# Kernel optimization log

Hardware: AMD Instinct MI355X
Metric: run time of the kernel (lower is better)

## Reference

```python
import jax, jax.numpy as jnp
import numpy as np

B, SQ, SK, D, H = 4, 2048, 2048, 1024, 16
HD = D // H


def setup_inputs() -> dict:
    key = jax.random.key(0)
    ks = jax.random.split(key, 12)
    s = 1.0 / np.sqrt(D)
    return {
        "query": jax.random.normal(ks[0], (B, SQ, D), jnp.float32),
        "key": jax.random.normal(ks[1], (B, SK, D), jnp.float32),
        "value": jax.random.normal(ks[2], (B, SK, D), jnp.float32),
        "key_padding_mask": jax.random.randint(ks[3], (B, SK), 0, 2, jnp.int32),
        "Wq": jax.random.uniform(ks[4], (D, D), jnp.float32, -s, s),
        "bq": jnp.zeros((D,), jnp.float32),
        "Wk": jax.random.uniform(ks[5], (D, D), jnp.float32, -s, s),
        "bk": jnp.zeros((D,), jnp.float32),
        "Wv": jax.random.uniform(ks[6], (D, D), jnp.float32, -s, s),
        "bv": jnp.zeros((D,), jnp.float32),
        "Wo": jax.random.uniform(ks[7], (D, D), jnp.float32, -s, s),
        "bo": jnp.zeros((D,), jnp.float32),
    }


def reference(query, key, value, key_padding_mask, Wq, bq, Wk, bk, Wv, bv, Wo, bo):
    scale = HD ** -0.5
    # projections: torch Linear is x @ W.T + b
    q = (query @ Wq.T + bq).reshape(B, SQ, H, HD).transpose(0, 2, 1, 3)  # [B,H,SQ,HD]
    k = (key @ Wk.T + bk).reshape(B, SK, H, HD).transpose(0, 2, 1, 3)    # [B,H,SK,HD]
    v = (value @ Wv.T + bv).reshape(B, SK, H, HD).transpose(0, 2, 1, 3)  # [B,H,SK,HD]
    scores = jnp.einsum("bhqd,bhkd->bhqk", q, k) * scale                  # [B,H,SQ,SK]
    mask = key_padding_mask[:, None, None, :] != 0                        # True = keep
    scores = jnp.where(mask, scores, -jnp.inf)
    attn = jax.nn.softmax(scores, axis=-1)
    # dropout is identity at inference (eval mode)
    out = jnp.einsum("bhqk,bhkd->bhqd", attn, v)                          # [B,H,SQ,HD]
    out = out.transpose(0, 2, 1, 3).reshape(B, SQ, D)
    return out @ Wo.T + bo
```

## Files before the change

### kernel.cpp

```cpp
#include <hip/hip_runtime.h>


typedef __bf16 bf16_t;
typedef __attribute__((ext_vector_type(4))) __bf16 bf16x4;
typedef __attribute__((ext_vector_type(8))) __bf16 bf16x8;
typedef __attribute__((ext_vector_type(4))) float f32x4;

#define MFMA16(a, b, c) __builtin_amdgcn_mfma_f32_16x16x32_bf16(a, b, c, 0, 0, 0)

__device__ __forceinline__ void gl_lds16(const void* g, void* l) {
  __builtin_amdgcn_global_load_lds(
      (const __attribute__((address_space(1))) unsigned int*)g,
      (__attribute__((address_space(3))) unsigned int*)l, 16, 0, 0);
}

__global__ void wconv_kernel(const float* __restrict__ Wq, const float* __restrict__ Wk,
                             const float* __restrict__ Wv, const float* __restrict__ Wo,
                             bf16_t* __restrict__ out) {
  const int m = blockIdx.y;
  const float* src = (m == 0) ? Wq : (m == 1) ? Wk : (m == 2) ? Wv : Wo;
  bf16_t* dst = out + (size_t)m * (1024 * 1024);
  const int idx = (blockIdx.x * 256 + threadIdx.x) * 4;
  float4 v = *(const float4*)(src + idx);
  bf16x4 pk;
  pk[0] = (bf16_t)v.x; pk[1] = (bf16_t)v.y; pk[2] = (bf16_t)v.z; pk[3] = (bf16_t)v.w;
  *(bf16x4*)(dst + idx) = pk;
}

__global__ void iconv_kernel(const float* __restrict__ src, bf16_t* __restrict__ dst) {
  const size_t idx = ((size_t)blockIdx.x * 256 + threadIdx.x) * 4;
  float4 v = *(const float4*)(src + idx);
  bf16x4 pk;
  pk[0] = (bf16_t)v.x; pk[1] = (bf16_t)v.y; pk[2] = (bf16_t)v.z; pk[3] = (bf16_t)v.w;
  *(bf16x4*)(dst + idx) = pk;
}

__global__ __launch_bounds__(256, 2) void gemm_kernel(
    const bf16_t* __restrict__ A, const bf16_t* __restrict__ Bw,
    const float* __restrict__ bias, void* __restrict__ outp, const int out_mode) {
  __shared__ __align__(16) bf16_t As[2][16 * 512];
  __shared__ __align__(16) bf16_t Bs[2][16 * 512];

  const int tid = threadIdx.x;
  const int lane = tid & 63, wave = tid >> 6;
  const int fm = lane & 15, quad = lane >> 4;
  const int wr = wave >> 1, wc = wave & 1;
  const int m0 = blockIdx.x * 128, n0 = blockIdx.y * 128;

  f32x4 acc[4][4];
#pragma unroll
  for (int i = 0; i < 4; ++i)
#pragma unroll
    for (int j = 0; j < 4; ++j) acc[i][j] = f32x4{0.f, 0.f, 0.f, 0.f};

  auto stage = [&](int ks, int buf) {
    const int k0 = ks * 64;
#pragma unroll
    for (int it = 0; it < 4; ++it) {
      const int fid = wave * 4 + it;
      const int row = (fid >> 1) * 16 + fm;
      const int col = (fid & 1) * 32 + quad * 8;
      gl_lds16(A + (size_t)(m0 + row) * 1024 + k0 + col, As[buf] + fid * 512);
    }
#pragma unroll
    for (int it = 0; it < 4; ++it) {
      const int fid = wave * 4 + it;
      const int row = (fid >> 1) * 16 + fm;
      const int col = (fid & 1) * 32 + quad * 8;
      gl_lds16(Bw + (size_t)(n0 + row) * 1024 + k0 + col, Bs[buf] + fid * 512);
    }
  };

  stage(0, 0);
  for (int ks = 0; ks < 16; ++ks) {
    __syncthreads();
    if (ks + 1 < 16) stage(ks + 1, (ks + 1) & 1);
    const bf16_t* Ab = As[ks & 1];
    const bf16_t* Bb = Bs[ks & 1];
#pragma unroll
    for (int u = 0; u < 2; ++u) {
      bf16x8 af[4], bfr[4];
#pragma unroll
      for (int i = 0; i < 4; ++i)
        af[i] = *(const bf16x8*)(Ab + ((4 * wr + i) * 2 + u) * 512 + lane * 8);
#pragma unroll
      for (int j = 0; j < 4; ++j)
        bfr[j] = *(const bf16x8*)(Bb + ((4 * wc + j) * 2 + u) * 512 + lane * 8);
#pragma unroll
      for (int i = 0; i < 4; ++i)
#pragma unroll
        for (int j = 0; j < 4; ++j) acc[i][j] = MFMA16(af[i], bfr[j], acc[i][j]);
    }
  }

  float bval[4];
#pragma unroll
  for (int j = 0; j < 4; ++j) bval[j] = bias[n0 + wc * 64 + j * 16 + fm];

#pragma unroll
  for (int i = 0; i < 4; ++i) {
#pragma unroll
    for (int j = 0; j < 4; ++j) {
      const int col = n0 + wc * 64 + j * 16 + fm;
#pragma unroll
      for (int r = 0; r < 4; ++r) {
        const int row = m0 + wr * 64 + i * 16 + quad * 4 + r;
        const float v = acc[i][j][r] + bval[j];
        if (out_mode == 2) {
          ((float*)outp)[(size_t)row * 1024 + col] = v;
        } else if (out_mode == 0) {
          ((bf16_t*)outp)[(size_t)row * 1024 + col] = (bf16_t)v;
        } else {
          const int bb = row >> 11, sk = row & 2047;
          const int tt = sk >> 7, L128 = sk & 127;
          const int c = L128 >> 5, hf = (L128 >> 4) & 1;
          const int qd = (L128 >> 2) & 3, rr = L128 & 3;
          const int hh = col >> 6, hd = col & 63;
          const int nt = hd >> 4, fv = hd & 15;
          const size_t idx = (((size_t)(bb * 16 + hh)) << 17) + tt * 8192 +
                             (nt * 4 + c) * 512 + (qd * 16 + fv) * 8 + hf * 4 + rr;
          ((bf16_t*)outp)[idx] = (bf16_t)v;
        }
      }
    }
  }
}

__global__ __launch_bounds__(256, 2) void attn_kernel(
    const bf16_t* __restrict__ q16, const bf16_t* __restrict__ k16,
    const bf16_t* __restrict__ vt16, const int* __restrict__ mask,
    bf16_t* __restrict__ o16) {
  __shared__ __align__(16) bf16_t Kb[2][8192];
  __shared__ __align__(16) bf16_t Vb[2][8192];
  __shared__ float mbuf[2][128];
  __shared__ float lbuf[128];

  const int tid = threadIdx.x;
  const int lane = tid & 63, wave = tid >> 6;
  const int fm = lane & 15, quad = lane >> 4;
  const int lin = blockIdx.y * 16 + blockIdx.x;
  const int xcd = lin & 7, slot = lin >> 3;
  const int qt = slot & 15;
  const int bh = ((slot >> 4) << 3) + xcd;
  const int b = bh >> 4, h = bh & 15;
  const float SC = 0.125f * 1.44269504f;

  bf16x8 aq[2][2];
#pragma unroll
  for (int i = 0; i < 2; ++i)
#pragma unroll
    for (int dc = 0; dc < 2; ++dc) {
      const int row = qt * 128 + (2 * wave + i) * 16 + fm;
      aq[i][dc] = *(const bf16x8*)(q16 + ((size_t)(b * 2048 + row)) * 1024 + h * 64 +
                                   dc * 32 + quad * 8);
    }

  auto stageKV = [&](int t, int buf) {
    const bf16_t* kb = k16 + ((size_t)(b * 2048 + t * 128)) * 1024 + h * 64;
#pragma unroll
    for (int s = 0; s < 4; ++s) {
      const int fid = wave * 4 + s;
      const int row = (fid >> 1) * 16 + fm;
      const int col = (fid & 1) * 32 + quad * 8;
      gl_lds16(kb + (size_t)row * 1024 + col, Kb[buf] + fid * 512);
    }
    const bf16_t* vbase = vt16 + ((size_t)bh << 17) + t * 8192;
#pragma unroll
    for (int s = 0; s < 4; ++s) {
      const int fid = wave * 4 + s;
      gl_lds16(vbase + fid * 512 + lane * 8, Vb[buf] + fid * 512);
    }
    if (tid < 128) mbuf[buf][tid] = mask[b * 2048 + t * 128 + tid] ? 0.0f : -1e30f;
  };

  f32x4 oacc[2][4];
#pragma unroll
  for (int i = 0; i < 2; ++i)
#pragma unroll
    for (int n = 0; n < 4; ++n) oacc[i][n] = f32x4{0.f, 0.f, 0.f, 0.f};
  float lrow[2] = {0.f, 0.f};

  stageKV(0, 0);
  for (int t = 0; t < 16; ++t) {
    __syncthreads();
    if (t + 1 < 16) stageKV(t + 1, (t + 1) & 1);
    const bf16_t* K = Kb[t & 1];
    const bf16_t* V = Vb[t & 1];
    const float* mb = mbuf[t & 1];

    f32x4 sacc[2][8];
#pragma unroll
    for (int i = 0; i < 2; ++i)
#pragma unroll
      for (int j = 0; j < 8; ++j) sacc[i][j] = f32x4{0.f, 0.f, 0.f, 0.f};
#pragma unroll
    for (int j = 0; j < 8; ++j) {
#pragma unroll
      for (int dc = 0; dc < 2; ++dc) {
        bf16x8 kf = *(const bf16x8*)(K + (j * 2 + dc) * 512 + lane * 8);
        sacc[0][j] = MFMA16(kf, aq[0][dc], sacc[0][j]);
        sacc[1][j] = MFMA16(kf, aq[1][dc], sacc[1][j]);
      }
    }

#pragma unroll
    for (int j = 0; j < 8; ++j) {
      f32x4 md = *(const f32x4*)&mb[j * 16 + quad * 4];
#pragma unroll
      for (int i = 0; i < 2; ++i) {
#pragma unroll
        for (int r = 0; r < 4; ++r) {
          const float p = __builtin_amdgcn_exp2f(fmaf(sacc[i][j][r], SC, md[r]));
          sacc[i][j][r] = p;
          lrow[i] += p;
        }
      }
    }

#pragma unroll
    for (int c = 0; c < 4; ++c) {
      bf16x8 pf[2];
#pragma unroll
      for (int i = 0; i < 2; ++i) {
#pragma unroll
        for (int r = 0; r < 4; ++r) {
          pf[i][r] = (bf16_t)sacc[i][2 * c][r];
          pf[i][4 + r] = (bf16_t)sacc[i][2 * c + 1][r];
        }
      }
#pragma unroll
      for (int n = 0; n < 4; ++n) {
        bf16x8 vv = *(const bf16x8*)(V + (n * 4 + c) * 512 + lane * 8);
        oacc[0][n] = MFMA16(pf[0], vv, oacc[0][n]);
        oacc[1][n] = MFMA16(pf[1], vv, oacc[1][n]);
      }
    }
  }

#pragma unroll
  for (int i = 0; i < 2; ++i) {
    float l = lrow[i];
    l += __shfl_xor(l, 16);
    l += __shfl_xor(l, 32);
    if (quad == 0) lbuf[wave * 32 + i * 16 + fm] = l;
  }
  __syncthreads();
#pragma unroll
  for (int i = 0; i < 2; ++i) {
    f32x4 lv = *(const f32x4*)&lbuf[wave * 32 + i * 16 + quad * 4];
#pragma unroll
    for (int r = 0; r < 4; ++r) {
      const float inv = 1.0f / lv[r];
      const int row = qt * 128 + wave * 32 + i * 16 + quad * 4 + r;
#pragma unroll
      for (int n = 0; n < 4; ++n) {
        o16[((size_t)(b * 2048 + row)) * 1024 + h * 64 + n * 16 + fm] =
            (bf16_t)(oacc[i][n][r] * inv);
      }
    }
  }
}

extern "C" void kernel_launch(void* const* d_in, const int* in_sizes, int n_in,
                              void* d_out, int out_size, void* d_ws, size_t ws_size,
                              hipStream_t stream) {
  const float* query = (const float*)d_in[0];
  const float* key   = (const float*)d_in[1];
  const float* value = (const float*)d_in[2];
  const int* mask    = (const int*)d_in[3];
  const float* Wq = (const float*)d_in[4];
  const float* bq = (const float*)d_in[5];
  const float* Wk = (const float*)d_in[6];
  const float* bk = (const float*)d_in[7];
  const float* Wv = (const float*)d_in[8];
  const float* bv = (const float*)d_in[9];
  const float* Wo = (const float*)d_in[10];
  const float* bo = (const float*)d_in[11];

  const size_t MB = 1024 * 1024;
  char* ws = (char*)d_ws;
  bf16_t* W16     = (bf16_t*)ws;
  bf16_t* q16     = (bf16_t*)(ws + 8 * MB);
  bf16_t* k16     = (bf16_t*)(ws + 24 * MB);
  bf16_t* vt16    = (bf16_t*)(ws + 40 * MB);
  bf16_t* scratch = (bf16_t*)(ws + 56 * MB);

  wconv_kernel<<<dim3(1024, 4), 256, 0, stream>>>(Wq, Wk, Wv, Wo, W16);

  iconv_kernel<<<8192, 256, 0, stream>>>(query, scratch);
  gemm_kernel<<<dim3(64, 8), 256, 0, stream>>>(scratch, W16,           bq, q16,  0);

  iconv_kernel<<<8192, 256, 0, stream>>>(key, scratch);
  gemm_kernel<<<dim3(64, 8), 256, 0, stream>>>(scratch, W16 + 1048576, bk, k16,  0);

  iconv_kernel<<<8192, 256, 0, stream>>>(value, scratch);
  gemm_kernel<<<dim3(64, 8), 256, 0, stream>>>(scratch, W16 + 2097152, bv, vt16, 1);

  attn_kernel<<<dim3(16, 64), 256, 0, stream>>>(q16, k16, vt16, mask, scratch);

  gemm_kernel<<<dim3(64, 8), 256, 0, stream>>>(scratch, W16 + 3145728, bo, d_out, 2);
}
```

Baseline: 433.0 us.

## Deepen GEMM load pipeline to four stages with manual vmcnt waits

Replaces the double-buffered 64-wide K staging in the projection GEMM with a four-buffer ring of 32-wide K slices, keeping three stages of global-to-LDS loads in flight. It uses explicit s_waitcnt vmcnt counts and a raw s_barrier instead of __syncthreads, which would otherwise drain every outstanding load. The aim is to hide global memory latency behind MFMA work. In exchange the loop runs twice as many iterations with half the MFMAs per barrier, and the hand-written wait counts must exactly match the number of loads issued per stage.

After: 415.5 us. 1.04x faster.

```diff
diff --git a/kernel.cpp b/kernel.cpp
--- a/kernel.cpp
+++ b/kernel.cpp
@@ -8,10 +8,18 @@
 
 #define MFMA16(a, b, c) __builtin_amdgcn_mfma_f32_16x16x32_bf16(a, b, c, 0, 0, 0)
 
+#define WAITV(N) asm volatile("s_waitcnt vmcnt(" #N ")" ::: "memory")
+
 __device__ __forceinline__ void gl_lds16(const void* g, void* l) {
   __builtin_amdgcn_global_load_lds(
       (const __attribute__((address_space(1))) unsigned int*)g,
       (__attribute__((address_space(3))) unsigned int*)l, 16, 0, 0);
+}
+
+__device__ __forceinline__ void block_barrier() {
+  asm volatile("" ::: "memory");
+  __builtin_amdgcn_s_barrier();
+  asm volatile("" ::: "memory");
 }
 
 __global__ void wconv_kernel(const float* __restrict__ Wq, const float* __restrict__ Wk,
@@ -38,8 +46,8 @@
 __global__ __launch_bounds__(256, 2) void gemm_kernel(
     const bf16_t* __restrict__ A, const bf16_t* __restrict__ Bw,
     const float* __restrict__ bias, void* __restrict__ outp, const int out_mode) {
-  __shared__ __align__(16) bf16_t As[2][16 * 512];
-  __shared__ __align__(16) bf16_t Bs[2][16 * 512];
+  __shared__ __align__(16) bf16_t As[4][8 * 512];
+  __shared__ __align__(16) bf16_t Bs[4][8 * 512];
 
   const int tid = threadIdx.x;
   const int lane = tid & 63, wave = tid >> 6;
@@ -54,43 +62,47 @@
     for (int j = 0; j < 4; ++j) acc[i][j] = f32x4{0.f, 0.f, 0.f, 0.f};
 
   auto stage = [&](int ks, int buf) {
-    const int k0 = ks * 64;
-#pragma unroll
-    for (int it = 0; it < 4; ++it) {
-      const int fid = wave * 4 + it;
-      const int row = (fid >> 1) * 16 + fm;
-      const int col = (fid & 1) * 32 + quad * 8;
-      gl_lds16(A + (size_t)(m0 + row) * 1024 + k0 + col, As[buf] + fid * 512);
-    }
-#pragma unroll
-    for (int it = 0; it < 4; ++it) {
-      const int fid = wave * 4 + it;
-      const int row = (fid >> 1) * 16 + fm;
-      const int col = (fid & 1) * 32 + quad * 8;
-      gl_lds16(Bw + (size_t)(n0 + row) * 1024 + k0 + col, Bs[buf] + fid * 512);
+    const int k0 = ks * 32;
+#pragma unroll
+    for (int it = 0; it < 2; ++it) {
+      const int fid = wave * 2 + it;
+      gl_lds16(A + (size_t)(m0 + fid * 16 + fm) * 1024 + k0 + quad * 8,
+               As[buf] + fid * 512);
+    }
+#pragma unroll
+    for (int it = 0; it < 2; ++it) {
+      const int fid = wave * 2 + it;
+      gl_lds16(Bw + (size_t)(n0 + fid * 16 + fm) * 1024 + k0 + quad * 8,
+               Bs[buf] + fid * 512);
     }
   };
 
   stage(0, 0);
-  for (int ks = 0; ks < 16; ++ks) {
-    __syncthreads();
-    if (ks + 1 < 16) stage(ks + 1, (ks + 1) & 1);
-    const bf16_t* Ab = As[ks & 1];
-    const bf16_t* Bb = Bs[ks & 1];
-#pragma unroll
-    for (int u = 0; u < 2; ++u) {
-      bf16x8 af[4], bfr[4];
-#pragma unroll
-      for (int i = 0; i < 4; ++i)
-        af[i] = *(const bf16x8*)(Ab + ((4 * wr + i) * 2 + u) * 512 + lane * 8);
-#pragma unroll
-      for (int j = 0; j < 4; ++j)
-        bfr[j] = *(const bf16x8*)(Bb + ((4 * wc + j) * 2 + u) * 512 + lane * 8);
-#pragma unroll
-      for (int i = 0; i < 4; ++i)
-#pragma unroll
-        for (int j = 0; j < 4; ++j) acc[i][j] = MFMA16(af[i], bfr[j], acc[i][j]);
-    }
+  stage(1, 1);
+  stage(2, 2);
+  for (int ks = 0; ks < 32; ++ks) {
+    if (ks <= 29) {
+      WAITV(8);
+    } else if (ks == 30) {
+      WAITV(4);
+    } else {
+      WAITV(0);
+    }
+    block_barrier();
+    if (ks + 3 < 32) stage(ks + 3, (ks + 3) & 3);
+    const bf16_t* Ab = As[ks & 3];
+    const bf16_t* Bb = Bs[ks & 3];
+    bf16x8 af[4], bfr[4];
+#pragma unroll
+    for (int i = 0; i < 4; ++i)
+      af[i] = *(const bf16x8*)(Ab + (4 * wr + i) * 512 + lane * 8);
+#pragma unroll
+    for (int j = 0; j < 4; ++j)
+      bfr[j] = *(const bf16x8*)(Bb + (4 * wc + j) * 512 + lane * 8);
+#pragma unroll
+    for (int i = 0; i < 4; ++i)
+#pragma unroll
+      for (int j = 0; j < 4; ++j) acc[i][j] = MFMA16(af[i], bfr[j], acc[i][j]);
   }
 
   float bval[4];
```
